# Performance work log

Hardware: AMD Instinct MI355X
Metric: run time of the kernel (lower is better)

Reference implementation:

```python
import jax, jax.numpy as jnp
import numpy as np

N, E, R, D = 50000, 800000, 12, 64


def setup_inputs() -> dict:
    key = jax.random.key(0)
    ks = jax.random.split(key, 32)
    s = 0.1
    inp = {
        'x': jnp.ones((N, 1), jnp.float32),
        'src': jax.random.randint(ks[0], (E,), 0, N, dtype=jnp.int32),
        'dst': jax.random.randint(ks[1], (E,), 0, N, dtype=jnp.int32),
        'etype': jax.random.randint(ks[2], (E,), 0, R, dtype=jnp.int32),
        'W_emb': s * jax.random.normal(ks[3], (1, D), jnp.float32),
        'b_emb': jnp.zeros((D,), jnp.float32),
    }
    i = 4
    for l in (1, 2, 3):
        inp[f'Wrel{l}'] = s * jax.random.normal(ks[i], (R, D, D), jnp.float32); i += 1
        inp[f'Wself{l}'] = s * jax.random.normal(ks[i], (D, D), jnp.float32); i += 1
        inp[f'b{l}'] = jnp.zeros((D,), jnp.float32)
        inp[f'gatew{l}'] = s * jax.random.normal(ks[i], (D,), jnp.float32); i += 1
        inp[f'gateb{l}'] = jnp.zeros((), jnp.float32)
        inp[f'attn{l}'] = s * jax.random.normal(ks[i], (D,), jnp.float32); i += 1
    inp['Wskip2'] = s * jax.random.normal(ks[i], (D, D), jnp.float32); i += 1
    inp['Wskip3'] = s * jax.random.normal(ks[i], (D, D), jnp.float32)
    return inp


def _segment_softmax(score, seg, n):
    m = jax.ops.segment_max(score, seg, num_segments=n)
    e = jnp.exp(score - m[seg])
    z = jax.ops.segment_sum(e, seg, num_segments=n)
    return e / (z[seg] + 1e-16)


def _rgcn_layer(h, src, dst, etype, Wrel, Wself, b, gw, gb, av, skip_h=None, Wskip=None, act=True):
    n = h.shape[0]
    # transform nodes under every relation, then gather per-edge: avoids [E,din,dout] weight gather
    msgs_all = jnp.einsum('nd,rde->nre', h, Wrel)          # [N,R,dout]
    m = msgs_all[src, etype]                               # [E,dout]
    gate = jax.nn.sigmoid(m @ gw + gb)                     # [E] edge gate
    score = jax.nn.leaky_relu(m @ av)                      # [E] attention logit
    alpha = _segment_softmax(score, dst, n)                # softmax over incoming edges
    m = m * (gate * alpha)[:, None]
    out = jax.ops.segment_sum(m, dst, num_segments=n) + h @ Wself + b
    if skip_h is not None:
        out = out + skip_h @ Wskip
    return jax.nn.relu(out) if act else out


def reference(x, src, dst, etype, W_emb, b_emb,
              Wrel1, Wself1, b1, gatew1, gateb1, attn1,
              Wrel2, Wself2, b2, gatew2, gateb2, attn2,
              Wrel3, Wself3, b3, gatew3, gateb3, attn3,
              Wskip2, Wskip3):
    h0 = jax.nn.relu(x @ W_emb + b_emb)                    # embed layer, [N,D]
    h1 = _rgcn_layer(h0, src, dst, etype, Wrel1, Wself1, b1, gatew1, gateb1, attn1, act=True)
    h2 = _rgcn_layer(h1, src, dst, etype, Wrel2, Wself2, b2, gatew2, gateb2, attn2, h1, Wskip2, act=True)
    h3 = _rgcn_layer(h2, src, dst, etype, Wrel3, Wself3, b3, gatew3, gateb3, attn3, h2, Wskip3, act=False)
    return h3
```

## Files before the change

kernel.cpp:

```cpp
#include <hip/hip_runtime.h>

#define DD 64
#define RR 12
#define KTOT 832
#define NKS 26
#define ASTR 840
#define TROWS 16
#define EPB2 8192

typedef _Float16 half8v __attribute__((ext_vector_type(8)));
typedef __attribute__((ext_vector_type(4))) float f32x4;

__global__ void k_sgw2(const float* __restrict__ x, const float* __restrict__ Wemb,
                       const float* __restrict__ bemb,
                       const float* __restrict__ q, const float* __restrict__ g,
                       const float* __restrict__ gb, float2* __restrict__ EW, int N) {
    __shared__ float We[DD], Be[DD], qs[RR * 65], gs[RR * 65];
    int tid = threadIdx.x;
    if (tid < DD) { We[tid] = Wemb[tid]; Be[tid] = bemb[tid]; }
    for (int i = tid; i < RR * DD; i += 256) {
        int r = i >> 6, c = i & 63;
        qs[r * 65 + c] = q[i];
        gs[r * 65 + c] = g[i];
    }
    __syncthreads();
    int t = blockIdx.x * 256 + tid;
    if (t >= N * RR) return;
    int n = t / RR, r = t - n * RR;
    float xv = x[n];
    const float* qp = qs + r * 65;
    const float* gp = gs + r * 65;
    float aq = 0.f, ag = 0.f;
#pragma unroll
    for (int d = 0; d < DD; d++) {
        float h = fmaf(xv, We[d], Be[d]);
        h = h > 0.f ? h : 0.f;
        aq = fmaf(h, qp[d], aq);
        ag = fmaf(h, gp[d], ag);
    }
    float sc = aq > 0.f ? aq : 0.01f * aq;
    float ev = expf(sc);
    float gate = 1.f / (1.f + expf(-(ag + gb[0])));
    EW[t] = make_float2(ev, ev * gate);
}

__global__ void k_ew(const unsigned* __restrict__ epk, const float2* __restrict__ EW,
                     float2* __restrict__ wz, int E) {
    int t = blockIdx.x * blockDim.x + threadIdx.x;
    if (t >= E) return;
    unsigned pk = epk[t];
    int s = (int)(pk & 0xFFFFu);
    int e = (int)((pk >> 16) & 15u);
    wz[t] = EW[(size_t)s * RR + e];
}


__global__ void k_bh(const int* __restrict__ dst, int* __restrict__ bcnt,
                     int E, int nbuck) {
    __shared__ int lh[512];
    int tid = threadIdx.x;
    for (int i = tid; i < 512; i += 512) lh[i] = 0;
    __syncthreads();
    int base = blockIdx.x * EPB2;
    int lim = base + EPB2 < E ? base + EPB2 : E;
    for (int i = base + tid; i < lim; i += 512)
        atomicAdd(&lh[dst[i] >> 7], 1);
    __syncthreads();
    for (int i = tid; i < nbuck; i += 512)
        if (lh[i]) atomicAdd(&bcnt[i], lh[i]);
}

__global__ void k_bscan(const int* __restrict__ bcnt, int* __restrict__ bbase,
                        int* __restrict__ bcur, int nbuck, int E) {
    __shared__ int wsum[8];
    int tid = threadIdx.x, lane = tid & 63, wv = tid >> 6;
    int v = (tid < nbuck) ? bcnt[tid] : 0;
    int incl = v;
#pragma unroll
    for (int d = 1; d < 64; d <<= 1) {
        int t2 = __shfl_up(incl, d);
        if (lane >= d) incl += t2;
    }
    if (lane == 63) wsum[wv] = incl;
    __syncthreads();
    int pre = 0;
#pragma unroll
    for (int w = 0; w < 8; w++) if (w < wv) pre += wsum[w];
    int excl = pre + incl - v;
    if (tid < nbuck) { bbase[tid] = excl; bcur[tid] = excl; }
    if (tid == nbuck - 1) bbase[nbuck] = excl + v;
}

__global__ void k_bscat(const int* __restrict__ src, const int* __restrict__ dst,
                        const int* __restrict__ et, int* __restrict__ bcur,
                        unsigned* __restrict__ epk2, int E, int nbuck) {
    __shared__ int lh[512];
    __shared__ int lcur[512];
    int tid = threadIdx.x;
    for (int i = tid; i < 512; i += 512) lh[i] = 0;
    __syncthreads();
    int base = blockIdx.x * EPB2;
    int lim = base + EPB2 < E ? base + EPB2 : E;
    for (int i = base + tid; i < lim; i += 512)
        atomicAdd(&lh[dst[i] >> 7], 1);
    __syncthreads();
    for (int i = tid; i < nbuck; i += 512)
        lcur[i] = lh[i] ? atomicAdd(&bcur[i], lh[i]) : 0;
    __syncthreads();
    for (int i = base + tid; i < lim; i += 512) {
        int d = dst[i];
        int pos = atomicAdd(&lcur[d >> 7], 1);
        epk2[pos] = ((unsigned)(d & 127) << 20) | ((unsigned)et[i] << 16) | (unsigned)src[i];
    }
}

__global__ void k_b2(const unsigned* __restrict__ epk2, const int* __restrict__ bbase,
                     unsigned* __restrict__ epk, int* __restrict__ offd,
                     int N, int E) {
    int b = blockIdx.x, tid = threadIdx.x;
    int p0 = bbase[b], p1 = bbase[b + 1], cb = p1 - p0;
    __shared__ int hist[1536];
    __shared__ int cur[1536];
    __shared__ int nodeTot[128], nodeExcl[128];
    __shared__ int wsum1;
    __shared__ unsigned stg[4096];
    for (int i = tid; i < 1536; i += 256) hist[i] = 0;
    __syncthreads();
    for (int i = tid; i < cb; i += 256) {
        unsigned pk = epk2[p0 + i];
        int key = (int)((pk >> 20) & 127u) * 12 + (int)((pk >> 16) & 15u);
        atomicAdd(&hist[key], 1);
    }
    __syncthreads();
    int incl = 0, v = 0;
    if (tid < 128) {
        int base = tid * 12, s = 0;
#pragma unroll
        for (int j = 0; j < 12; j++) { int c = hist[base + j]; hist[base + j] = s; s += c; }
        nodeTot[tid] = s;
        v = s; incl = s;
        int lane = tid & 63;
#pragma unroll
        for (int d = 1; d < 64; d <<= 1) {
            int t2 = __shfl_up(incl, d);
            if (lane >= d) incl += t2;
        }
        if (tid == 63) wsum1 = incl;
    }
    __syncthreads();
    if (tid < 128) {
        int pre = (tid >= 64) ? wsum1 : 0;
        nodeExcl[tid] = pre + incl - v;
    }
    __syncthreads();
    if (tid < 128) {
        int node = b * 128 + tid;
        int base = tid * 12;
        if (node < N) offd[node] = p0 + nodeExcl[tid];
#pragma unroll
        for (int j = 0; j < 12; j++) cur[base + j] = nodeExcl[tid] + hist[base + j];
    }
    if (b == 0 && tid == 0) offd[N] = E;
    __syncthreads();
    if (cb <= 4096) {
        for (int i = tid; i < cb; i += 256) {
            unsigned pk = epk2[p0 + i];
            int key = (int)((pk >> 20) & 127u) * 12 + (int)((pk >> 16) & 15u);
            int pos = atomicAdd(&cur[key], 1);
            stg[pos] = pk & 0xFFFFFu;
        }
        __syncthreads();
        for (int i = tid; i < cb; i += 256) epk[p0 + i] = stg[i];
    } else {
        for (int i = tid; i < cb; i += 256) {
            unsigned pk = epk2[p0 + i];
            int key = (int)((pk >> 20) & 127u) * 12 + (int)((pk >> 16) & 15u);
            int pos = atomicAdd(&cur[key], 1);
            epk[p0 + pos] = pk & 0xFFFFFu;
        }
    }
}

__global__ void k_wprep3(
    const float* __restrict__ Wr0, const float* __restrict__ Ws0, const float* __restrict__ Wk0,
    const float* __restrict__ av0, const float* __restrict__ gw0,
    _Float16* __restrict__ Bh0, _Float16* __restrict__ Bl0, float* __restrict__ q0, float* __restrict__ g0,
    const float* __restrict__ Wr1, const float* __restrict__ Ws1, const float* __restrict__ Wk1,
    const float* __restrict__ av1, const float* __restrict__ gw1,
    _Float16* __restrict__ Bh1, _Float16* __restrict__ Bl1, float* __restrict__ q1, float* __restrict__ g1,
    const float* __restrict__ Wr2, const float* __restrict__ Ws2, const float* __restrict__ Wk2,
    const float* __restrict__ av2, const float* __restrict__ gw2,
    _Float16* __restrict__ Bh2, _Float16* __restrict__ Bl2, float* __restrict__ q2, float* __restrict__ g2) {
    int layer = blockIdx.x / (NKS + 3);
    int bx = blockIdx.x % (NKS + 3);
    const float* Wrel  = layer == 0 ? Wr0 : layer == 1 ? Wr1 : Wr2;
    const float* Wself = layer == 0 ? Ws0 : layer == 1 ? Ws1 : Ws2;
    const float* Wskip = layer == 0 ? Wk0 : layer == 1 ? Wk1 : Wk2;
    const float* av    = layer == 0 ? av0 : layer == 1 ? av1 : av2;
    const float* gw    = layer == 0 ? gw0 : layer == 1 ? gw1 : gw2;
    _Float16* Bh = layer == 0 ? Bh0 : layer == 1 ? Bh1 : Bh2;
    _Float16* Bl = layer == 0 ? Bl0 : layer == 1 ? Bl1 : Bl2;
    float* q = layer == 0 ? q0 : layer == 1 ? q1 : q2;
    float* g = layer == 0 ? g0 : layer == 1 ? g1 : g2;

    if (bx < NKS) {
        int t = bx * 256 + threadIdx.x;
        int ks = t >> 8, ct = (t >> 6) & 3, lane = t & 63;
        int col = ct * 16 + (lane & 15);
        int kb = ks * 32 + ((lane >> 4) << 3);
        _Float16* ph = Bh + (size_t)t * 8;
        _Float16* pl = Bl + (size_t)t * 8;
#pragma unroll
        for (int i = 0; i < 8; i++) {
            int k = kb + i;
            float v;
            if (k < 768) v = Wrel[(size_t)k * DD + col];
            else {
                v = Wself[(size_t)(k - 768) * DD + col];
                if (Wskip) v += Wskip[(size_t)(k - 768) * DD + col];
            }
            _Float16 h = (_Float16)v;
            ph[i] = h;
            pl[i] = (_Float16)(v - (float)h);
        }
    } else {
        int t = (bx - NKS) * 256 + threadIdx.x;
        if (t >= RR * DD) return;
        const float* wp = Wrel + (size_t)t * DD;
        float aq = 0.f, ag = 0.f;
#pragma unroll
        for (int e = 0; e < DD; e++) { float w = wp[e]; aq += w * av[e]; ag += w * gw[e]; }
        q[t] = aq; g[t] = ag;
    }
}

template<int NB, bool MASKED, int XD>
__device__ __forceinline__ void ebatch(const unsigned* __restrict__ epk,
                                       const float2* __restrict__ wz,
                                       const _Float16* __restrict__ hin16,
                                       const float* __restrict__ xsrc,
                                       float we_r, float be_r,
                                       int p, int p1, int lane,
                                       _Float16* wav, float& zacc,
                                       int& cur_e, float& racc) {
    int len = p1 - p;
    unsigned pk[NB];
    float2 ew[NB];
#pragma unroll
    for (int i = 0; i < NB; i++) {
        int ii = MASKED ? (i < len ? i : len - 1) : i;
        pk[i] = epk[p + ii];
    }
#pragma unroll
    for (int i = 0; i < NB; i++) {
        int ii = MASKED ? (i < len ? i : len - 1) : i;
        ew[i] = wz[p + ii];
    }
    if (XD) {
        float xs[NB];
#pragma unroll
        for (int i = 0; i < NB; i++) xs[i] = xsrc[pk[i] & 0xFFFFu];
        __builtin_amdgcn_sched_barrier(0);
#pragma unroll
        for (int i = 0; i < NB; i++) {
            int e = __builtin_amdgcn_readfirstlane((int)((pk[i] >> 16) & 15u));
            if (e != cur_e) {
                wav[cur_e * 64 + lane] = (_Float16)racc;
                racc = 0.f;
                cur_e = e;
            }
            float hh = fmaf(xs[i], we_r, be_r);
            hh = hh > 0.f ? hh : 0.f;
            float wx = ew[i].x, wy = ew[i].y;
            if (MASKED && i >= 1) {
                bool ok = i < len;
                wx = ok ? wx : 0.f;
                wy = ok ? wy : 0.f;
            }
            zacc += wx;
            racc = fmaf(wy, hh, racc);
        }
    } else {
        _Float16 hr[NB];
#pragma unroll
        for (int i = 0; i < NB; i++)
            hr[i] = hin16[(size_t)(pk[i] & 0xFFFFu) * DD + lane];
        __builtin_amdgcn_sched_barrier(0);
#pragma unroll
        for (int i = 0; i < NB; i++) {
            int e = __builtin_amdgcn_readfirstlane((int)((pk[i] >> 16) & 15u));
            if (e != cur_e) {
                wav[cur_e * 64 + lane] = (_Float16)racc;
                racc = 0.f;
                cur_e = e;
            }
            float hh = (float)hr[i];
            float wx = ew[i].x, wy = ew[i].y;
            if (MASKED && i >= 1) {
                bool ok = i < len;
                wx = ok ? wx : 0.f;
                wy = ok ? wy : 0.f;
            }
            zacc += wx;
            racc = fmaf(wy, hh, racc);
        }
    }
}

template<int XD>
__global__ void __launch_bounds__(512, 8)
k_fused(const unsigned* __restrict__ epk, const int* __restrict__ offd,
        const _Float16* __restrict__ hin16,
        const float* __restrict__ xsrc, const float* __restrict__ Wemb,
        const float* __restrict__ bemb,
        const float2* __restrict__ wz, float2* __restrict__ EWw,
        const _Float16* __restrict__ Bh, const _Float16* __restrict__ Bl,
        const float* __restrict__ bias, float* __restrict__ out,
        _Float16* __restrict__ hout16, int N, int act,
        const float* __restrict__ qn, const float* __restrict__ gn,
        const float* __restrict__ gbn) {
    __shared__ __align__(16) _Float16 At[TROWS * ASTR];
    __shared__ __align__(16) _Float16 pool16[8 * RR * 64];
    __shared__ int offs[TROWS + 1];
    __shared__ int claim;
    int tid = threadIdx.x, lane = tid & 63, w = tid >> 6;
    int nb0 = blockIdx.x * TROWS;
    if (tid == 0) claim = 0;
    if (tid < TROWS + 1) {
        int nn = nb0 + tid;
        offs[tid] = (nn <= N) ? offd[nn] : 0;
    }
    float we_r = 0.f, be_r = 0.f;
    if (XD) { we_r = Wemb[lane]; be_r = bemb[lane]; }
    __syncthreads();

    _Float16* wav = pool16 + w * (RR * 64);

    for (;;) {
        int t0 = 0;
        if (lane == 0) t0 = atomicAdd(&claim, 1);
        int nl = __builtin_amdgcn_readfirstlane(t0);
        if (nl >= TROWS) break;
        int node = nb0 + nl;
        _Float16* Ar = At + nl * ASTR;
        if (node >= N) {
            for (int k = lane; k < KTOT; k += 64) Ar[k] = (_Float16)0.f;
            continue;
        }
        int p0 = __builtin_amdgcn_readfirstlane(offs[nl]);
        int p1 = __builtin_amdgcn_readfirstlane(offs[nl + 1]);

#pragma unroll
        for (int r = 0; r < RR; r++) wav[r * 64 + lane] = (_Float16)0.f;
        float zacc = 0.f;
        float racc = 0.f;
        int cur_e = (p0 < p1) ? (int)(__builtin_amdgcn_readfirstlane(
                        (int)((epk[p0] >> 16) & 15u))) : 0;
        int p = p0;
        while (p + 16 <= p1) {
            ebatch<16, false, XD>(epk, wz, hin16, xsrc, we_r, be_r, p, p1, lane,
                                  wav, zacc, cur_e, racc);
            p += 16;
        }
        int rem = p1 - p;
        if (rem > 8)      ebatch<16, true, XD>(epk, wz, hin16, xsrc, we_r, be_r, p, p1, lane,
                                               wav, zacc, cur_e, racc);
        else if (rem > 0) ebatch<8, true, XD>(epk, wz, hin16, xsrc, we_r, be_r, p, p1, lane,
                                              wav, zacc, cur_e, racc);
        wav[cur_e * 64 + lane] = (_Float16)racc;

        float inv = 1.f / (zacc + 1e-16f);
#pragma unroll
        for (int r = 0; r < RR; r++)
            Ar[r * DD + lane] = (_Float16)((float)wav[r * 64 + lane] * inv);
        if (XD) {
            float h0v = fmaf(xsrc[node], we_r, be_r);
            h0v = h0v > 0.f ? h0v : 0.f;
            Ar[768 + lane] = (_Float16)h0v;
        } else {
            Ar[768 + lane] = hin16[(size_t)node * DD + lane];
        }
    }
    __syncthreads();

    float* Hf = (float*)pool16;
    float* qg = (float*)pool16 + 1088;

    if (w < 4) {
        const half8v* Bh8 = (const half8v*)Bh;
        const half8v* Bl8 = (const half8v*)Bl;
        const _Float16* abase = At + (lane & 15) * ASTR + ((lane >> 4) << 3);
        f32x4 acc0 = {0.f, 0.f, 0.f, 0.f};
#pragma unroll 4
        for (int ks = 0; ks < NKS; ++ks) {
            half8v ah = *(const half8v*)(abase + ks * 32);
            size_t bb = (size_t)(ks * 4 + w) * 64 + lane;
            half8v bh = Bh8[bb];
            half8v bl = Bl8[bb];
            acc0 = __builtin_amdgcn_mfma_f32_16x16x32_f16(ah, bh, acc0, 0, 0, 0);
            acc0 = __builtin_amdgcn_mfma_f32_16x16x32_f16(ah, bl, acc0, 0, 0, 0);
        }

        int colb = lane & 15, kg = lane >> 4;
        int c = w * 16 + colb;
        float bv = bias[c];
#pragma unroll
        for (int j = 0; j < 4; j++) {
            int rl = kg * 4 + j;
            int row = nb0 + rl;
            if (row < N) {
                float v = acc0[j] + bv;
                if (act) v = v > 0.f ? v : 0.f;
                if (out) out[(size_t)row * DD + c] = v;
                if (hout16) hout16[(size_t)row * DD + c] = (_Float16)v;
                if (EWw) Hf[rl * 68 + c] = v;
            }
        }
    } else if (EWw) {
        for (int i = tid - 256; i < RR * DD; i += 256) {
            int r = i >> 6, c = i & 63;
            qg[r * 68 + c] = qn[i];
            qg[816 + r * 68 + c] = gn[i];
        }
    }

    if (EWw) {
        __syncthreads();
        if (tid < TROWS * RR) {
            int nl = tid / RR, r = tid - nl * RR;
            int node = nb0 + nl;
            if (node < N) {
                const float* hp = Hf + nl * 68;
                const float* qp = qg + r * 68;
                const float* gp = qg + 816 + r * 68;
                float aq = 0.f, ag = 0.f;
#pragma unroll
                for (int c4 = 0; c4 < 16; c4++) {
                    float4 hv = *(const float4*)(hp + c4 * 4);
                    float4 qv = *(const float4*)(qp + c4 * 4);
                    float4 gv = *(const float4*)(gp + c4 * 4);
                    aq += hv.x * qv.x + hv.y * qv.y + hv.z * qv.z + hv.w * qv.w;
                    ag += hv.x * gv.x + hv.y * gv.y + hv.z * gv.z + hv.w * gv.w;
                }
                float sc = aq > 0.f ? aq : 0.01f * aq;
                float ev = expf(sc);
                float gate = 1.f / (1.f + expf(-(ag + gbn[0])));
                EWw[(size_t)node * RR + r] = make_float2(ev, ev * gate);
            }
        }
    }
}

extern "C" void kernel_launch(void* const* d_in, const int* in_sizes, int n_in,
                              void* d_out, int out_size, void* d_ws, size_t ws_size,
                              hipStream_t stream) {
    const float* x    = (const float*)d_in[0];
    const int*   src  = (const int*)d_in[1];
    const int*   dst  = (const int*)d_in[2];
    const int*   etyp = (const int*)d_in[3];
    const float* Wemb = (const float*)d_in[4];
    const float* bemb = (const float*)d_in[5];
    const int N = in_sizes[0];
    const int E = in_sizes[1];
    const int nbuck = (N + 127) >> 7;
    const int nblk2 = (E + EPB2 - 1) / EPB2;

    const float* Wrel[3];  const float* Wself[3]; const float* bb[3];
    const float* gwv[3];   const float* gbv[3];   const float* av[3];
    for (int l = 0; l < 3; l++) {
        int o = 6 + 6 * l;
        Wrel[l]  = (const float*)d_in[o + 0];
        Wself[l] = (const float*)d_in[o + 1];
        bb[l]    = (const float*)d_in[o + 2];
        gwv[l]   = (const float*)d_in[o + 3];
        gbv[l]   = (const float*)d_in[o + 4];
        av[l]    = (const float*)d_in[o + 5];
    }
    const float* Wskip[3] = { nullptr, (const float*)d_in[24], (const float*)d_in[25] };

    float* p = (float*)d_ws;
    _Float16* h16A = (_Float16*)p; p += (size_t)N * DD / 2;
    _Float16* h16B = (_Float16*)p; p += (size_t)N * DD / 2;
    float2* EWa = (float2*)p; p += (size_t)N * RR * 2;
    float2* EWb = (float2*)p; p += (size_t)N * RR * 2;
    float2* wzv = (float2*)p; p += (size_t)E * 2;
    float* qv3[3]; float* gv3[3]; _Float16* Bh3[3]; _Float16* Bl3[3];
    for (int l = 0; l < 3; l++) {
        qv3[l] = p; p += RR * DD;
        gv3[l] = p; p += RR * DD;
        Bh3[l] = (_Float16*)p; p += NKS * 4 * 64 * 8 / 2;
        Bl3[l] = (_Float16*)p; p += NKS * 4 * 64 * 8 / 2;
    }
    unsigned* epk2 = (unsigned*)p; p += E;
    unsigned* epk  = (unsigned*)p; p += E;
    int* bcnt  = (int*)p; p += 512;
    int* bbase = (int*)p; p += 516;
    int* bcur  = (int*)p; p += 512;
    int* offd  = (int*)p; p += N + 4;

    const int B = 256;

    k_wprep3<<<3 * (NKS + 3), B, 0, stream>>>(
        Wrel[0], Wself[0], Wskip[0], av[0], gwv[0], Bh3[0], Bl3[0], qv3[0], gv3[0],
        Wrel[1], Wself[1], Wskip[1], av[1], gwv[1], Bh3[1], Bl3[1], qv3[1], gv3[1],
        Wrel[2], Wself[2], Wskip[2], av[2], gwv[2], Bh3[2], Bl3[2], qv3[2], gv3[2]);

    hipMemsetAsync(bcnt, 0, 512 * 4, stream);
    k_bh<<<nblk2, 512, 0, stream>>>(dst, bcnt, E, nbuck);
    k_bscan<<<1, 512, 0, stream>>>(bcnt, bbase, bcur, nbuck, E);
    k_bscat<<<nblk2, 512, 0, stream>>>(src, dst, etyp, bcur, epk2, E, nbuck);
    k_b2<<<nbuck, 256, 0, stream>>>(epk2, bbase, epk, offd, N, E);

    k_sgw2<<<(N * RR + B - 1) / B, B, 0, stream>>>(x, Wemb, bemb, qv3[0], gv3[0],
                                                   gbv[0], EWa, N);

    const int fblocks = (N + TROWS - 1) / TROWS;
    const int eblocks = (E + B - 1) / B;

    k_ew<<<eblocks, B, 0, stream>>>(epk, EWa, wzv, E);
    k_fused<1><<<fblocks, 512, 0, stream>>>(epk, offd, nullptr, x, Wemb, bemb,
                                            wzv, EWb, Bh3[0], Bl3[0], bb[0],
                                            nullptr, h16B, N, 1,
                                            qv3[1], gv3[1], gbv[1]);
    k_ew<<<eblocks, B, 0, stream>>>(epk, EWb, wzv, E);
    k_fused<0><<<fblocks, 512, 0, stream>>>(epk, offd, h16B, nullptr, nullptr, nullptr,
                                            wzv, EWa, Bh3[1], Bl3[1], bb[1],
                                            nullptr, h16A, N, 1,
                                            qv3[2], gv3[2], gbv[2]);
    k_ew<<<eblocks, B, 0, stream>>>(epk, EWa, wzv, E);
    k_fused<0><<<fblocks, 512, 0, stream>>>(epk, offd, h16A, nullptr, nullptr, nullptr,
                                            wzv, nullptr, Bh3[2], Bl3[2], bb[2],
                                            (float*)d_out, nullptr, N, 0,
                                            nullptr, nullptr, nullptr);
}
```

Before: 225.6 us.

## Scatter per-edge weights directly from node producers, dropping the k_ew gather passes

Builds a second sort of the dst-sorted edges, keyed by (src node, relation), which gives a CSR (offd2) and a position list (spos) mapping back to dst-sorted slots. The node-level softmax/gate producers (initial kernel and the fused layer epilogue) then write each node-relation weight straight into the per-edge array, removing the three separate k_ew gather kernels and the N*R intermediate. This adds a second bucket sort (histogram, scan, scatter, local sort) in preprocessing, and the writes become random scatters done by a few threads per block, which may serialize on high-degree entries.

```diff
diff --git a/kernel.cpp b/kernel.cpp
--- a/kernel.cpp
+++ b/kernel.cpp
@@ -11,10 +11,13 @@
 typedef _Float16 half8v __attribute__((ext_vector_type(8)));
 typedef __attribute__((ext_vector_type(4))) float f32x4;
 
-__global__ void k_sgw2(const float* __restrict__ x, const float* __restrict__ Wemb,
-                       const float* __restrict__ bemb,
-                       const float* __restrict__ q, const float* __restrict__ g,
-                       const float* __restrict__ gb, float2* __restrict__ EW, int N) {
+__global__ void k_sgw2s(const float* __restrict__ x, const float* __restrict__ Wemb,
+                        const float* __restrict__ bemb,
+                        const float* __restrict__ q, const float* __restrict__ g,
+                        const float* __restrict__ gb,
+                        const unsigned* __restrict__ spos,
+                        const int* __restrict__ offd2,
+                        float2* __restrict__ wz, int N) {
     __shared__ float We[DD], Be[DD], qs[RR * 65], gs[RR * 65];
     int tid = threadIdx.x;
     if (tid < DD) { We[tid] = Wemb[tid]; Be[tid] = bemb[tid]; }
@@ -41,17 +44,10 @@
     float sc = aq > 0.f ? aq : 0.01f * aq;
     float ev = expf(sc);
     float gate = 1.f / (1.f + expf(-(ag + gb[0])));
-    EW[t] = make_float2(ev, ev * gate);
-}
-
-__global__ void k_ew(const unsigned* __restrict__ epk, const float2* __restrict__ EW,
-                     float2* __restrict__ wz, int E) {
-    int t = blockIdx.x * blockDim.x + threadIdx.x;
-    if (t >= E) return;
-    unsigned pk = epk[t];
-    int s = (int)(pk & 0xFFFFu);
-    int e = (int)((pk >> 16) & 15u);
-    wz[t] = EW[(size_t)s * RR + e];
+    float2 v = make_float2(ev, ev * gate);
+    int o0 = offd2[(size_t)n * RR + r];
+    int o1 = offd2[(size_t)n * RR + r + 1];
+    for (int p2 = o0; p2 < o1; ++p2) wz[spos[p2]] = v;
 }
 
 
@@ -177,6 +173,116 @@
             int key = (int)((pk >> 20) & 127u) * 12 + (int)((pk >> 16) & 15u);
             int pos = atomicAdd(&cur[key], 1);
             epk[p0 + pos] = pk & 0xFFFFFu;
+        }
+    }
+}
+
+
+__global__ void k_bhs(const unsigned* __restrict__ epk, int* __restrict__ bcnt,
+                      int E, int nbuck) {
+    __shared__ int lh[512];
+    int tid = threadIdx.x;
+    for (int i = tid; i < 512; i += 512) lh[i] = 0;
+    __syncthreads();
+    int base = blockIdx.x * EPB2;
+    int lim = base + EPB2 < E ? base + EPB2 : E;
+    for (int i = base + tid; i < lim; i += 512)
+        atomicAdd(&lh[(epk[i] & 0xFFFFu) >> 7], 1);
+    __syncthreads();
+    for (int i = tid; i < nbuck; i += 512)
+        if (lh[i]) atomicAdd(&bcnt[i], lh[i]);
+}
+
+__global__ void k_bscats(const unsigned* __restrict__ epk, int* __restrict__ bcur,
+                         unsigned* __restrict__ spk2, int E, int nbuck) {
+    __shared__ int lh[512];
+    __shared__ int lcur[512];
+    int tid = threadIdx.x;
+    for (int i = tid; i < 512; i += 512) lh[i] = 0;
+    __syncthreads();
+    int base = blockIdx.x * EPB2;
+    int lim = base + EPB2 < E ? base + EPB2 : E;
+    for (int i = base + tid; i < lim; i += 512)
+        atomicAdd(&lh[(epk[i] & 0xFFFFu) >> 7], 1);
+    __syncthreads();
+    for (int i = tid; i < nbuck; i += 512)
+        lcur[i] = lh[i] ? atomicAdd(&bcur[i], lh[i]) : 0;
+    __syncthreads();
+    for (int i = base + tid; i < lim; i += 512) {
+        unsigned pk = epk[i];
+        int s = (int)(pk & 0xFFFFu);
+        int pos = atomicAdd(&lcur[s >> 7], 1);
+        spk2[pos] = ((unsigned)(s & 127) << 25) | (((pk >> 16) & 15u) << 21) | (unsigned)i;
+    }
+}
+
+__global__ void k_b2s(const unsigned* __restrict__ spk2, const int* __restrict__ bbase,
+                      unsigned* __restrict__ spos, int* __restrict__ offd2,
+                      int N, int E) {
+    int b = blockIdx.x, tid = threadIdx.x;
+    int p0 = bbase[b], p1 = bbase[b + 1], cb = p1 - p0;
+    __shared__ int hist[1536];
+    __shared__ int cur[1536];
+    __shared__ int nodeTot[128], nodeExcl[128];
+    __shared__ int wsum1;
+    __shared__ unsigned stg[4096];
+    for (int i = tid; i < 1536; i += 256) hist[i] = 0;
+    __syncthreads();
+    for (int i = tid; i < cb; i += 256) {
+        unsigned pk = spk2[p0 + i];
+        int key = (int)(pk >> 25) * 12 + (int)((pk >> 21) & 15u);
+        atomicAdd(&hist[key], 1);
+    }
+    __syncthreads();
+    int incl = 0, v = 0;
+    if (tid < 128) {
+        int base = tid * 12, s = 0;
+#pragma unroll
+        for (int j = 0; j < 12; j++) { int c = hist[base + j]; hist[base + j] = s; s += c; }
+        nodeTot[tid] = s;
+        v = s; incl = s;
+        int lane = tid & 63;
+#pragma unroll
+        for (int d = 1; d < 64; d <<= 1) {
+            int t2 = __shfl_up(incl, d);
+            if (lane >= d) incl += t2;
+        }
+        if (tid == 63) wsum1 = incl;
+    }
+    __syncthreads();
+    if (tid < 128) {
+        int pre = (tid >= 64) ? wsum1 : 0;
+        nodeExcl[tid] = pre + incl - v;
+    }
+    __syncthreads();
+    if (tid < 128) {
+        int node = b * 128 + tid;
+        int base = tid * 12;
+        if (node < N) {
+#pragma unroll
+            for (int j = 0; j < 12; j++)
+                offd2[(size_t)node * 12 + j] = p0 + nodeExcl[tid] + hist[base + j];
+        }
+#pragma unroll
+        for (int j = 0; j < 12; j++) cur[base + j] = nodeExcl[tid] + hist[base + j];
+    }
+    if (b == 0 && tid == 0) offd2[(size_t)N * 12] = E;
+    __syncthreads();
+    if (cb <= 4096) {
+        for (int i = tid; i < cb; i += 256) {
+            unsigned pk = spk2[p0 + i];
+            int key = (int)(pk >> 25) * 12 + (int)((pk >> 21) & 15u);
+            int pos = atomicAdd(&cur[key], 1);
+            stg[pos] = pk & 0x1FFFFFu;
+        }
+        __syncthreads();
+        for (int i = tid; i < cb; i += 256) spos[p0 + i] = stg[i];
+    } else {
+        for (int i = tid; i < cb; i += 256) {
+            unsigned pk = spk2[p0 + i];
+            int key = (int)(pk >> 25) * 12 + (int)((pk >> 21) & 15u);
+            int pos = atomicAdd(&cur[key], 1);
+            spos[p0 + pos] = pk & 0x1FFFFFu;
         }
     }
 }
@@ -313,7 +419,9 @@
         const _Float16* __restrict__ hin16,
         const float* __restrict__ xsrc, const float* __restrict__ Wemb,
         const float* __restrict__ bemb,
-        const float2* __restrict__ wz, float2* __restrict__ EWw,
+        const float2* __restrict__ wz,
+        const unsigned* __restrict__ spos, const int* __restrict__ offd2,
+        float2* __restrict__ wzNext,
         const _Float16* __restrict__ Bh, const _Float16* __restrict__ Bl,
         const float* __restrict__ bias, float* __restrict__ out,
         _Float16* __restrict__ hout16, int N, int act,
@@ -413,10 +521,10 @@
                 if (act) v = v > 0.f ? v : 0.f;
                 if (out) out[(size_t)row * DD + c] = v;
                 if (hout16) hout16[(size_t)row * DD + c] = (_Float16)v;
-                if (EWw) Hf[rl * 68 + c] = v;
+                if (wzNext) Hf[rl * 68 + c] = v;
             }
         }
-    } else if (EWw) {
+    } else if (wzNext) {
         for (int i = tid - 256; i < RR * DD; i += 256) {
             int r = i >> 6, c = i & 63;
             qg[r * 68 + c] = qn[i];
@@ -424,7 +532,7 @@
         }
     }
 
-    if (EWw) {
+    if (wzNext) {
         __syncthreads();
         if (tid < TROWS * RR) {
             int nl = tid / RR, r = tid - nl * RR;
@@ -445,7 +553,10 @@
                 float sc = aq > 0.f ? aq : 0.01f * aq;
                 float ev = expf(sc);
                 float gate = 1.f / (1.f + expf(-(ag + gbn[0])));
-                EWw[(size_t)node * RR + r] = make_float2(ev, ev * gate);
+                float2 v = make_float2(ev, ev * gate);
+                int o0 = offd2[(size_t)node * RR + r];
+                int o1 = offd2[(size_t)node * RR + r + 1];
+                for (int p2 = o0; p2 < o1; ++p2) wzNext[spos[p2]] = v;
             }
         }
     }
@@ -481,9 +592,8 @@
     float* p = (float*)d_ws;
     _Float16* h16A = (_Float16*)p; p += (size_t)N * DD / 2;
     _Float16* h16B = (_Float16*)p; p += (size_t)N * DD / 2;
-    float2* EWa = (float2*)p; p += (size_t)N * RR * 2;
-    float2* EWb = (float2*)p; p += (size_t)N * RR * 2;
-    float2* wzv = (float2*)p; p += (size_t)E * 2;
+    float2* wzA = (float2*)p; p += (size_t)E * 2;
+    float2* wzB = (float2*)p; p += (size_t)E * 2;
     float* qv3[3]; float* gv3[3]; _Float16* Bh3[3]; _Float16* Bl3[3];
     for (int l = 0; l < 3; l++) {
         qv3[l] = p; p += RR * DD;
@@ -493,6 +603,8 @@
     }
     unsigned* epk2 = (unsigned*)p; p += E;
     unsigned* epk  = (unsigned*)p; p += E;
+    unsigned* spos = (unsigned*)p; p += E;
+    int* offd2 = (int*)p; p += (size_t)N * RR + 4;
     int* bcnt  = (int*)p; p += 512;
     int* bbase = (int*)p; p += 516;
     int* bcur  = (int*)p; p += 512;
@@ -511,25 +623,30 @@
     k_bscat<<<nblk2, 512, 0, stream>>>(src, dst, etyp, bcur, epk2, E, nbuck);
     k_b2<<<nbuck, 256, 0, stream>>>(epk2, bbase, epk, offd, N, E);
 
-    k_sgw2<<<(N * RR + B - 1) / B, B, 0, stream>>>(x, Wemb, bemb, qv3[0], gv3[0],
-                                                   gbv[0], EWa, N);
+    hipMemsetAsync(bcnt, 0, 512 * 4, stream);
+    k_bhs<<<nblk2, 512, 0, stream>>>(epk, bcnt, E, nbuck);
+    k_bscan<<<1, 512, 0, stream>>>(bcnt, bbase, bcur, nbuck, E);
+    k_bscats<<<nblk2, 512, 0, stream>>>(epk, bcur, epk2, E, nbuck);
+    k_b2s<<<nbuck, 256, 0, stream>>>(epk2, bbase, spos, offd2, N, E);
+
+    k_sgw2s<<<(N * RR + B - 1) / B, B, 0, stream>>>(x, Wemb, bemb, qv3[0], gv3[0],
+                                                    gbv[0], spos, offd2, wzA, N);
 
     const int fblocks = (N + TROWS - 1) / TROWS;
-    const int eblocks = (E + B - 1) / B;
-
-    k_ew<<<eblocks, B, 0, stream>>>(epk, EWa, wzv, E);
+
     k_fused<1><<<fblocks, 512, 0, stream>>>(epk, offd, nullptr, x, Wemb, bemb,
-                                            wzv, EWb, Bh3[0], Bl3[0], bb[0],
+                                            wzA, spos, offd2, wzB,
+                                            Bh3[0], Bl3[0], bb[0],
                                             nullptr, h16B, N, 1,
                                             qv3[1], gv3[1], gbv[1]);
-    k_ew<<<eblocks, B, 0, stream>>>(epk, EWb, wzv, E);
     k_fused<0><<<fblocks, 512, 0, stream>>>(epk, offd, h16B, nullptr, nullptr, nullptr,
-                                            wzv, EWa, Bh3[1], Bl3[1], bb[1],
+                                            wzB, spos, offd2, wzA,
+                                            Bh3[1], Bl3[1], bb[1],
                                             nullptr, h16A, N, 1,
                                             qv3[2], gv3[2], gbv[2]);
-    k_ew<<<eblocks, B, 0, stream>>>(epk, EWa, wzv, E);
     k_fused<0><<<fblocks, 512, 0, stream>>>(epk, offd, h16A, nullptr, nullptr, nullptr,
-                                            wzv, nullptr, Bh3[2], Bl3[2], bb[2],
+                                            wzA, nullptr, nullptr, nullptr,
+                                            Bh3[2], Bl3[2], bb[2],
                                             (float*)d_out, nullptr, N, 0,
                                             nullptr, nullptr, nullptr);
 }
```

New measurement: 244.5 us. 8.4% more time.
